# Performance work log

Measured on AMD Instinct MI355X. Metric: run time of the kernel, lower is better.

Reference implementation:

```python
import jax, jax.numpy as jnp
import numpy as np


def setup_inputs() -> dict:
    key = jax.random.key(0)
    k1, k2 = jax.random.split(key)
    B, N, T, D = 16, 2048, 168, 64
    spatial_nodes = jax.random.normal(k1, (B, N, D), dtype=jnp.float32)
    temporal_nodes = jax.random.normal(k2, (B, T, D), dtype=jnp.float32)
    return {"spatial_nodes": spatial_nodes, "temporal_nodes": temporal_nodes}


def reference(spatial_nodes, temporal_nodes):
    # node_embs: [B, N+T, D]
    node_embs = jnp.concatenate([spatial_nodes, temporal_nodes], axis=1)
    # Dense pairwise similarity, then tanh(relu(.)) threshold.
    # batch_adj: [B, N+T, N+T]
    batch_adj = jnp.einsum('bnf,bmf->bnm', node_embs, node_embs)
    batch_adj = jnp.tanh(jax.nn.relu(batch_adj))
    # The torch module additionally extracts per-batch variable-length
    # edge lists (nonzero indices + weights) from batch_adj; those are a
    # pure re-indexing of batch_adj with data-dependent shapes, so the
    # jit-compatible reference returns the dense adjacency, from which
    # edge lists are trivially recoverable (nonzero entries of batch_adj).
    return batch_adj
```

## Files before the change

### kernel.cpp

```cpp
#include <hip/hip_runtime.h>
#include <stdint.h>


constexpr int Bsz = 16;
constexpr int Nsp = 2048;
constexpr int Ttm = 168;
constexpr int D   = 64;
constexpr int M   = Nsp + Ttm;
constexpr int TILE = 128;
constexpr int LROW = 72;

typedef __attribute__((ext_vector_type(8)))  short bf16x8;
typedef __attribute__((ext_vector_type(16))) float f32x16;

__device__ inline void split_bf16(float x, unsigned short& h, unsigned short& l) {
    union { float f; uint32_t u; } a; a.f = x;
    uint32_t hu = (a.u + 0x7FFFu + ((a.u >> 16) & 1u)) >> 16;
    h = (unsigned short)hu;
    union { uint32_t u; float f; } hf; hf.u = hu << 16;
    union { float f; uint32_t u; } r; r.f = x - hf.f;
    uint32_t lu = (r.u + 0x7FFFu + ((r.u >> 16) & 1u)) >> 16;
    l = (unsigned short)lu;
}

__global__ __launch_bounds__(256, 2) void stgraph_kernel(
    const float* __restrict__ spatial,
    const float* __restrict__ temporal,
    float* __restrict__ out)
{
    __shared__ __align__(16) unsigned short Ah[TILE * LROW];
    __shared__ __align__(16) unsigned short Al[TILE * LROW];
    __shared__ __align__(16) unsigned short Bh[TILE * LROW];
    __shared__ __align__(16) unsigned short Bl[TILE * LROW];

    const int tid    = threadIdx.x;
    const int tile_j = blockIdx.x;
    const int tile_i = blockIdx.y;
    const int b      = blockIdx.z;

    const float* sp_b = spatial  + (size_t)b * Nsp * D;
    const float* tp_b = temporal + (size_t)b * Ttm * D;

    #pragma unroll
    for (int it = 0; it < 8; ++it) {
        const int f4  = tid + 256 * it;
        const int row = f4 >> 4;
        const int c4  = f4 & 15;
        {
            const int gi = tile_i * TILE + row;
            float4 v = make_float4(0.f, 0.f, 0.f, 0.f);
            if (gi < M) {
                const float* src = (gi < Nsp) ? (sp_b + (size_t)gi * D)
                                              : (tp_b + (size_t)(gi - Nsp) * D);
                v = *(const float4*)(src + c4 * 4);
            }
            unsigned short h[4], l[4];
            split_bf16(v.x, h[0], l[0]); split_bf16(v.y, h[1], l[1]);
            split_bf16(v.z, h[2], l[2]); split_bf16(v.w, h[3], l[3]);
            *(uint2*)(&Ah[row * LROW + c4 * 4]) = *(const uint2*)h;
            *(uint2*)(&Al[row * LROW + c4 * 4]) = *(const uint2*)l;
        }
        {
            const int gj = tile_j * TILE + row;
            float4 v = make_float4(0.f, 0.f, 0.f, 0.f);
            if (gj < M) {
                const float* src = (gj < Nsp) ? (sp_b + (size_t)gj * D)
                                              : (tp_b + (size_t)(gj - Nsp) * D);
                v = *(const float4*)(src + c4 * 4);
            }
            unsigned short h[4], l[4];
            split_bf16(v.x, h[0], l[0]); split_bf16(v.y, h[1], l[1]);
            split_bf16(v.z, h[2], l[2]); split_bf16(v.w, h[3], l[3]);
            *(uint2*)(&Bh[row * LROW + c4 * 4]) = *(const uint2*)h;
            *(uint2*)(&Bl[row * LROW + c4 * 4]) = *(const uint2*)l;
        }
    }
    __syncthreads();

    const int lane = tid & 63;
    const int w    = tid >> 6;
    const int l31  = lane & 31;
    const int lhi  = lane >> 5;
    const int arow = 32 * w + l31;

    f32x16 acc[4] = {};

    #pragma unroll
    for (int ks = 0; ks < 4; ++ks) {
        const int ko = ks * 16 + 8 * lhi;
        bf16x8 ahi = *(const bf16x8*)(&Ah[arow * LROW + ko]);
        bf16x8 alo = *(const bf16x8*)(&Al[arow * LROW + ko]);
        #pragma unroll
        for (int t = 0; t < 4; ++t) {
            const int brow = 32 * t + l31;
            bf16x8 bhi = *(const bf16x8*)(&Bh[brow * LROW + ko]);
            bf16x8 blo = *(const bf16x8*)(&Bl[brow * LROW + ko]);
            acc[t] = __builtin_amdgcn_mfma_f32_32x32x16_bf16(ahi, bhi, acc[t], 0, 0, 0);
            acc[t] = __builtin_amdgcn_mfma_f32_32x32x16_bf16(ahi, blo, acc[t], 0, 0, 0);
            acc[t] = __builtin_amdgcn_mfma_f32_32x32x16_bf16(alo, bhi, acc[t], 0, 0, 0);
        }
    }

    float* out_b = out + (size_t)b * M * M;
    #pragma unroll
    for (int t = 0; t < 4; ++t) {
        const int gj = tile_j * TILE + 32 * t + l31;
        if (gj >= M) continue;
        #pragma unroll
        for (int r = 0; r < 16; ++r) {
            const int lrow = (r & 3) + 8 * (r >> 2) + 4 * lhi;
            const int gi = tile_i * TILE + 32 * w + lrow;
            if (gi >= M) continue;
            const float x = fmaxf(acc[t][r], 0.0f);
            const float e = __expf(2.0f * x);
            const float v = 1.0f - 2.0f / (e + 1.0f);
            out_b[(size_t)gi * M + gj] = v;
        }
    }
}

extern "C" void kernel_launch(void* const* d_in, const int* in_sizes, int n_in,
                              void* d_out, int out_size, void* d_ws, size_t ws_size,
                              hipStream_t stream) {
    const float* spatial  = (const float*)d_in[0];
    const float* temporal = (const float*)d_in[1];
    float* out = (float*)d_out;

    dim3 block(256);
    dim3 grid((M + TILE - 1) / TILE, (M + TILE - 1) / TILE, Bsz);
    stgraph_kernel<<<grid, block, 0, stream>>>(spatial, temporal, out);
}
```

Measured before the change: 467.0 us.

## Exploit Gram-matrix symmetry: compute upper-triangle tiles and write transposed copy

Launches only upper-triangular tile pairs per batch, decoding the pair index into tile coordinates. Each off-diagonal block computes its tile once and writes both it and its transpose, staging the transpose through shared memory for coalesced float4 stores. Diagonal blocks load a single operand tile. This halves MFMA work and input loading, but output write volume is unchanged, and extra LDS traffic and syncs are added.

```diff
diff --git a/kernel.cpp b/kernel.cpp
--- a/kernel.cpp
+++ b/kernel.cpp
@@ -8,7 +8,10 @@
 constexpr int D   = 64;
 constexpr int M   = Nsp + Ttm;
 constexpr int TILE = 128;
+constexpr int NT   = (M + TILE - 1) / TILE;
+constexpr int NPAIR = NT * (NT + 1) / 2;
 constexpr int LROW = 72;
+constexpr int TROW = 132;
 
 typedef __attribute__((ext_vector_type(8)))  short bf16x8;
 typedef __attribute__((ext_vector_type(16))) float f32x16;
@@ -23,20 +26,33 @@
     l = (unsigned short)lu;
 }
 
+__device__ inline float act_tanh_relu(float x) {
+    const float xr = fmaxf(x, 0.0f);
+    const float e  = __expf(2.0f * xr);
+    return 1.0f - 2.0f / (e + 1.0f);
+}
+
 __global__ __launch_bounds__(256, 2) void stgraph_kernel(
     const float* __restrict__ spatial,
     const float* __restrict__ temporal,
     float* __restrict__ out)
 {
-    __shared__ __align__(16) unsigned short Ah[TILE * LROW];
-    __shared__ __align__(16) unsigned short Al[TILE * LROW];
-    __shared__ __align__(16) unsigned short Bh[TILE * LROW];
-    __shared__ __align__(16) unsigned short Bl[TILE * LROW];
+    __shared__ __align__(16) unsigned short pool[4 * TILE * LROW];
+    unsigned short* Ah = pool;
+    unsigned short* Al = pool + 1 * TILE * LROW;
+    unsigned short* Bh = pool + 2 * TILE * LROW;
+    unsigned short* Bl = pool + 3 * TILE * LROW;
+    float* T = (float*)pool;
 
-    const int tid    = threadIdx.x;
-    const int tile_j = blockIdx.x;
-    const int tile_i = blockIdx.y;
-    const int b      = blockIdx.z;
+    const int tid = threadIdx.x;
+    const int b   = blockIdx.y;
+
+    const int p = blockIdx.x;
+    int ti = (int)((37.0f - sqrtf(1369.0f - 8.0f * (float)p)) * 0.5f);
+    while (ti * (37 - ti) / 2 > p) --ti;
+    while ((ti + 1) * (36 - ti) / 2 <= p) ++ti;
+    const int tj = ti + (p - ti * (37 - ti) / 2);
+    const bool diag = (ti == tj);
 
     const float* sp_b = spatial  + (size_t)b * Nsp * D;
     const float* tp_b = temporal + (size_t)b * Ttm * D;
@@ -46,22 +62,26 @@
         const int f4  = tid + 256 * it;
         const int row = f4 >> 4;
         const int c4  = f4 & 15;
-        {
-            const int gi = tile_i * TILE + row;
-            float4 v = make_float4(0.f, 0.f, 0.f, 0.f);
-            if (gi < M) {
-                const float* src = (gi < Nsp) ? (sp_b + (size_t)gi * D)
-                                              : (tp_b + (size_t)(gi - Nsp) * D);
-                v = *(const float4*)(src + c4 * 4);
-            }
-            unsigned short h[4], l[4];
-            split_bf16(v.x, h[0], l[0]); split_bf16(v.y, h[1], l[1]);
-            split_bf16(v.z, h[2], l[2]); split_bf16(v.w, h[3], l[3]);
-            *(uint2*)(&Ah[row * LROW + c4 * 4]) = *(const uint2*)h;
-            *(uint2*)(&Al[row * LROW + c4 * 4]) = *(const uint2*)l;
+        const int gi  = ti * TILE + row;
+        float4 v = make_float4(0.f, 0.f, 0.f, 0.f);
+        if (gi < M) {
+            const float* src = (gi < Nsp) ? (sp_b + (size_t)gi * D)
+                                          : (tp_b + (size_t)(gi - Nsp) * D);
+            v = *(const float4*)(src + c4 * 4);
         }
-        {
-            const int gj = tile_j * TILE + row;
+        unsigned short h[4], l[4];
+        split_bf16(v.x, h[0], l[0]); split_bf16(v.y, h[1], l[1]);
+        split_bf16(v.z, h[2], l[2]); split_bf16(v.w, h[3], l[3]);
+        *(uint2*)(&Ah[row * LROW + c4 * 4]) = *(const uint2*)h;
+        *(uint2*)(&Al[row * LROW + c4 * 4]) = *(const uint2*)l;
+    }
+    if (!diag) {
+        #pragma unroll
+        for (int it = 0; it < 8; ++it) {
+            const int f4  = tid + 256 * it;
+            const int row = f4 >> 4;
+            const int c4  = f4 & 15;
+            const int gj  = tj * TILE + row;
             float4 v = make_float4(0.f, 0.f, 0.f, 0.f);
             if (gj < M) {
                 const float* src = (gj < Nsp) ? (sp_b + (size_t)gj * D)
@@ -76,6 +96,9 @@
         }
     }
     __syncthreads();
+
+    const unsigned short* FBh = diag ? Ah : Bh;
+    const unsigned short* FBl = diag ? Al : Bl;
 
     const int lane = tid & 63;
     const int w    = tid >> 6;
@@ -93,8 +116,8 @@
         #pragma unroll
         for (int t = 0; t < 4; ++t) {
             const int brow = 32 * t + l31;
-            bf16x8 bhi = *(const bf16x8*)(&Bh[brow * LROW + ko]);
-            bf16x8 blo = *(const bf16x8*)(&Bl[brow * LROW + ko]);
+            bf16x8 bhi = *(const bf16x8*)(&FBh[brow * LROW + ko]);
+            bf16x8 blo = *(const bf16x8*)(&FBl[brow * LROW + ko]);
             acc[t] = __builtin_amdgcn_mfma_f32_32x32x16_bf16(ahi, bhi, acc[t], 0, 0, 0);
             acc[t] = __builtin_amdgcn_mfma_f32_32x32x16_bf16(ahi, blo, acc[t], 0, 0, 0);
             acc[t] = __builtin_amdgcn_mfma_f32_32x32x16_bf16(alo, bhi, acc[t], 0, 0, 0);
@@ -102,19 +125,47 @@
     }
 
     float* out_b = out + (size_t)b * M * M;
+
+    if (!diag) __syncthreads();
+
     #pragma unroll
     for (int t = 0; t < 4; ++t) {
-        const int gj = tile_j * TILE + 32 * t + l31;
-        if (gj >= M) continue;
+        const int jl = 32 * t + l31;
+        const int gj = tj * TILE + jl;
+        float v[16];
         #pragma unroll
-        for (int r = 0; r < 16; ++r) {
-            const int lrow = (r & 3) + 8 * (r >> 2) + 4 * lhi;
-            const int gi = tile_i * TILE + 32 * w + lrow;
-            if (gi >= M) continue;
-            const float x = fmaxf(acc[t][r], 0.0f);
-            const float e = __expf(2.0f * x);
-            const float v = 1.0f - 2.0f / (e + 1.0f);
-            out_b[(size_t)gi * M + gj] = v;
+        for (int r = 0; r < 16; ++r) v[r] = act_tanh_relu(acc[t][r]);
+
+        if (gj < M) {
+            #pragma unroll
+            for (int r = 0; r < 16; ++r) {
+                const int gi = ti * TILE + 32 * w + (r & 3) + 8 * (r >> 2) + 4 * lhi;
+                if (gi < M) out_b[(size_t)gi * M + gj] = v[r];
+            }
+        }
+        if (!diag) {
+            #pragma unroll
+            for (int g = 0; g < 4; ++g) {
+                const int rowbase = 32 * w + 8 * g + 4 * lhi;
+                float4 w4 = make_float4(v[4 * g + 0], v[4 * g + 1],
+                                        v[4 * g + 2], v[4 * g + 3]);
+                *(float4*)(&T[jl * TROW + rowbase]) = w4;
+            }
+        }
+    }
+
+    if (!diag) {
+        __syncthreads();
+        #pragma unroll
+        for (int it = 0; it < 16; ++it) {
+            const int slot = tid + 256 * it;
+            const int jl   = slot >> 5;
+            const int c4   = slot & 31;
+            const int grow = tj * TILE + jl;
+            if (grow < M) {
+                float4 v4 = *(const float4*)(&T[jl * TROW + 4 * c4]);
+                *(float4*)(&out_b[(size_t)grow * M + ti * TILE + 4 * c4]) = v4;
+            }
         }
     }
 }
@@ -127,6 +178,6 @@
     float* out = (float*)d_out;
 
     dim3 block(256);
-    dim3 grid((M + TILE - 1) / TILE, (M + TILE - 1) / TILE, Bsz);
+    dim3 grid(NPAIR, Bsz);
     stgraph_kernel<<<grid, block, 0, stream>>>(spatial, temporal, out);
 }
```

After: 427.3 us. 1.09x faster.
